# Performance work log

Measured on AMD Instinct MI355X. Metric: run time of the kernel, lower is better.

## Reference

```python
import jax, jax.numpy as jnp
import numpy as np

NUM_EMBEDDINGS = 512
EMBEDDING_DIM = 128
COMMITMENT = 0.25
DECAY = 0.99
EPS = 1e-05


def setup_inputs() -> dict:
    key = jax.random.key(0)
    k1, k2 = jax.random.split(key)
    z = jax.random.normal(k1, (32, EMBEDDING_DIM, 64, 64), dtype=jnp.float32)
    embedding = jax.random.normal(k2, (EMBEDDING_DIM, NUM_EMBEDDINGS), dtype=jnp.float32)
    cluster_size = jnp.zeros((NUM_EMBEDDINGS,), dtype=jnp.float32)
    embed_avg = embedding  # buffer initialized as a clone of embedding
    return {"z": z, "embedding": embedding, "cluster_size": cluster_size, "embed_avg": embed_avg}


def reference(z, embedding, cluster_size, embed_avg):
    sg = jax.lax.stop_gradient
    D, K = embedding.shape
    B, C, H, W = z.shape
    z_perm = jnp.transpose(z, (0, 2, 3, 1))          # [B,H,W,D]
    flat_z = z_perm.reshape(-1, D)                    # [N,D]

    distances = ((flat_z ** 2).sum(1, keepdims=True)
                 - 2.0 * (flat_z @ embedding)
                 + (embedding ** 2).sum(0)[None, :])  # [N,K]
    idx = jnp.argmin(distances, axis=1)               # [N]

    # gather codes (equivalent to one-hot @ embedding.T, without materializing one-hot)
    quantized = jnp.take(embedding.T, idx, axis=0).reshape(z_perm.shape)  # [B,H,W,D]
    quantized = jnp.transpose(quantized, (0, 3, 1, 2))                    # [B,D,H,W]

    # EMA codebook update (training branch)
    enc_sum = jax.ops.segment_sum(jnp.ones_like(idx, dtype=flat_z.dtype), idx, num_segments=K)  # [K]
    embed_sum = jax.ops.segment_sum(flat_z, idx, num_segments=K).T                              # [D,K]
    new_cluster_size = cluster_size * DECAY + (1.0 - DECAY) * enc_sum
    new_embed_avg = embed_avg * DECAY + (1.0 - DECAY) * embed_sum
    n = jnp.maximum(new_cluster_size.sum(), 1e-05)
    cs = (new_cluster_size + EPS) / (n + K * EPS) * n
    new_embedding = new_embed_avg / cs[None, :]

    e_latent_loss = jnp.mean((sg(quantized) - z) ** 2)
    q_latent_loss = jnp.mean((quantized - sg(z)) ** 2)
    loss = q_latent_loss + COMMITMENT * e_latent_loss

    quantized_out = z + sg(quantized - z)             # straight-through
    encoding_indices = idx.reshape(B, H, W)
    return (quantized_out, loss, encoding_indices, new_embedding, new_cluster_size, new_embed_avg)
```

## Files before the change

### kernel.cpp

```cpp
#include <hip/hip_runtime.h>
#include <hip/hip_bf16.h>
#include <float.h>

typedef _Float16 f16;
typedef __attribute__((ext_vector_type(8))) _Float16 half8;
typedef __attribute__((ext_vector_type(4))) float floatx4;

#define DIM   128
#define HW    4096
#define NPOS  131072
#define K     512
#define ZSTRIDE_B 524288

#define Q_OFF     0
#define LOSS_OFF  16777216
#define IDX_OFF   16777217
#define NEMB_OFF  16908289
#define NCS_OFF   16973825
#define NEA_OFF   16974337

#define WS_LOSS  0
#define WS_E2    2
#define WS_ENC   514
#define WS_ESUM  1026
#define WS_ZERO_COUNT 66562
#define WS_EHI   66564
#define WS_ELO   99332

#define XST 136

__global__ __launch_bounds__(256) void k_prep(const float* __restrict__ emb,
                                              f16* __restrict__ ehiP,
                                              f16* __restrict__ eloP,
                                              float* __restrict__ e2) {
    int lin = blockIdx.x * 256 + threadIdx.x;
    int o = lin >> 9, k = lin & 511;
    int g = k >> 4, r = k & 15;
    half8 hh, ll;
    float s = 0.f;
    #pragma unroll
    for (int j = 0; j < 8; ++j) {
        float v = emb[(o * 8 + j) * K + k];
        f16 h = (f16)v;
        f16 l = (f16)(v - (float)h);
        hh[j] = h; ll[j] = l;
        s = fmaf(v, v, s);
    }
    int base = (g * 4 + (o >> 2)) * 512 + (o & 3) * 128 + r * 8;
    *(half8*)&ehiP[base] = hh;
    *(half8*)&eloP[base] = ll;
    unsafeAtomicAdd(&e2[k], s);
}

__global__ __launch_bounds__(256) void k_assign(const float* __restrict__ z,
                                                const f16* __restrict__ ehiP,
                                                const f16* __restrict__ eloP,
                                                const float* __restrict__ e2,
                                                float* __restrict__ out,
                                                float* __restrict__ lossAcc) {
    __shared__ f16 xs_h[64 * XST];
    __shared__ f16 xs_l[64 * XST];
    __shared__ float wbD[256];
    __shared__ int   wbI[256];
    __shared__ int   bidx[64];
    __shared__ float wred[4];

    const int tid  = threadIdx.x;
    const int lane = tid & 63;
    const int wv   = tid >> 6;
    const int n0   = blockIdx.x * 64;
    const int b    = n0 >> 12;
    const int hw0  = n0 & 4095;
    const float* zb = z + b * ZSTRIDE_B + hw0;
    const int l15  = lane & 15;
    const int quad = lane >> 4;

    float sv0[16], sv1[16];
    #pragma unroll
    for (int it = 0; it < 16; ++it) {
        int lin = tid + it * 256;
        int i  = lin & 63;
        int dp = lin >> 6;
        sv0[it] = zb[(2 * dp) * HW + i];
        sv1[it] = zb[(2 * dp + 1) * HW + i];
    }
    #pragma unroll
    for (int it = 0; it < 16; ++it) {
        int lin = tid + it * 256;
        int i  = lin & 63;
        int dp = lin >> 6;
        float v0 = sv0[it], v1 = sv1[it];
        f16 h0 = (f16)v0; f16 l0 = (f16)(v0 - (float)h0);
        f16 h1 = (f16)v1; f16 l1 = (f16)(v1 - (float)h1);
        union { f16 h[2]; unsigned int u; } ph, pl;
        ph.h[0] = h0; ph.h[1] = h1;
        pl.h[0] = l0; pl.h[1] = l1;
        *(unsigned int*)&xs_h[i * XST + 2 * dp] = ph.u;
        *(unsigned int*)&xs_l[i * XST + 2 * dp] = pl.u;
    }
    __syncthreads();

    float bestD[4][4];
    int   bestI[4][4];
    #pragma unroll
    for (int t = 0; t < 4; ++t)
        #pragma unroll
        for (int r = 0; r < 4; ++r) { bestD[t][r] = FLT_MAX; bestI[t][r] = 0x7fffffff; }

    const half8* gh = (const half8*)ehiP;
    const half8* gl = (const half8*)eloP;

    for (int cc = 0; cc < 4; ++cc) {
        half8 Bh[4][2], Bl[4][2];
        #pragma unroll
        for (int dc = 0; dc < 4; ++dc)
            #pragma unroll
            for (int nt = 0; nt < 2; ++nt) {
                int g  = cc * 8 + wv * 2 + nt;
                int bi = (g * 4 + dc) * 64 + lane;
                Bh[dc][nt] = gh[bi];
                Bl[dc][nt] = gl[bi];
            }

        floatx4 acc[4][2];
        #pragma unroll
        for (int t = 0; t < 4; ++t)
            #pragma unroll
            for (int nt = 0; nt < 2; ++nt) acc[t][nt] = (floatx4){0.f, 0.f, 0.f, 0.f};

        #pragma unroll
        for (int dc = 0; dc < 4; ++dc) {
            half8 ah[4], al[4];
            #pragma unroll
            for (int t = 0; t < 4; ++t) {
                int off = (t * 16 + l15) * XST + dc * 32 + quad * 8;
                ah[t] = *(const half8*)&xs_h[off];
                al[t] = *(const half8*)&xs_l[off];
            }
            #pragma unroll
            for (int nt = 0; nt < 2; ++nt) {
                #pragma unroll
                for (int t = 0; t < 4; ++t) {
                    acc[t][nt] = __builtin_amdgcn_mfma_f32_16x16x32_f16(ah[t], Bh[dc][nt], acc[t][nt], 0, 0, 0);
                    acc[t][nt] = __builtin_amdgcn_mfma_f32_16x16x32_f16(al[t], Bh[dc][nt], acc[t][nt], 0, 0, 0);
                    acc[t][nt] = __builtin_amdgcn_mfma_f32_16x16x32_f16(ah[t], Bl[dc][nt], acc[t][nt], 0, 0, 0);
                }
            }
        }
        #pragma unroll
        for (int nt = 0; nt < 2; ++nt) {
            int c = cc * 128 + wv * 32 + nt * 16 + l15;
            float ee = e2[c];
            #pragma unroll
            for (int t = 0; t < 4; ++t)
                #pragma unroll
                for (int r = 0; r < 4; ++r) {
                    float s = fmaf(-2.f, acc[t][nt][r], ee);
                    if (s < bestD[t][r]) { bestD[t][r] = s; bestI[t][r] = c; }
                }
        }
    }

    #pragma unroll
    for (int mask = 1; mask <= 8; mask <<= 1) {
        #pragma unroll
        for (int t = 0; t < 4; ++t)
            #pragma unroll
            for (int r = 0; r < 4; ++r) {
                float od = __shfl_xor(bestD[t][r], mask, 64);
                int   oi = __shfl_xor(bestI[t][r], mask, 64);
                if (od < bestD[t][r] || (od == bestD[t][r] && oi < bestI[t][r])) {
                    bestD[t][r] = od; bestI[t][r] = oi;
                }
            }
    }
    if (l15 == 0) {
        #pragma unroll
        for (int t = 0; t < 4; ++t)
            #pragma unroll
            for (int r = 0; r < 4; ++r) {
                int m = t * 16 + quad * 4 + r;
                wbD[wv * 64 + m] = bestD[t][r];
                wbI[wv * 64 + m] = bestI[t][r];
            }
    }
    __syncthreads();
    if (tid < 64) {
        float bd = wbD[tid]; int bi = wbI[tid];
        #pragma unroll
        for (int w = 1; w < 4; ++w) {
            float od = wbD[w * 64 + tid]; int oi = wbI[w * 64 + tid];
            if (od < bd || (od == bd && oi < bi)) { bd = od; bi = oi; }
        }
        bidx[tid] = bi;
        out[IDX_OFF + n0 + tid] = (float)bi;
    }
    __syncthreads();

    float* qb = out + Q_OFF + b * ZSTRIDE_B + hw0;
    float lsum = 0.f;
    #pragma unroll
    for (int it = 0; it < 4; ++it) {
        int o = wv * 4 + it;
        int c = bidx[lane];
        int g = c >> 4, r = c & 15;
        int base = (g * 4 + (o >> 2)) * 512 + (o & 3) * 128 + r * 8;
        half8 hh = *(const half8*)&ehiP[base];
        half8 ll = *(const half8*)&eloP[base];
        half8 zh = *(const half8*)&xs_h[lane * XST + o * 8];
        half8 zl = *(const half8*)&xs_l[lane * XST + o * 8];
        #pragma unroll
        for (int jj = 0; jj < 8; ++jj) {
            float q  = (float)hh[jj] + (float)ll[jj];
            float zz = (float)zh[jj] + (float)zl[jj];
            qb[(o * 8 + jj) * HW + lane] = q;
            float df = q - zz;
            lsum = fmaf(df, df, lsum);
        }
    }
    #pragma unroll
    for (int m = 32; m >= 1; m >>= 1) lsum += __shfl_xor(lsum, m, 64);
    if (lane == 0) wred[wv] = lsum;
    __syncthreads();
    if (tid == 0) unsafeAtomicAdd(lossAcc, wred[0] + wred[1] + wred[2] + wred[3]);
}

#define DC 8
__global__ __launch_bounds__(256) void k_ema2(const float* __restrict__ z,
                                              const float* __restrict__ out,
                                              float* __restrict__ enc,
                                              float* __restrict__ esum) {
    __shared__ float acc[DC][K];
    __shared__ float cnt[K];

    const int tid = threadIdx.x;
    const int half   = blockIdx.x & 1;
    const int dchunk = (blockIdx.x >> 1) & 15;
    const int b      = blockIdx.x >> 5;
    const int d0 = dchunk * DC;
    const bool doCnt = (dchunk == 0);

    for (int i = tid; i < DC * K; i += 256) ((float*)acc)[i] = 0.f;
    if (doCnt) for (int i = tid; i < K; i += 256) cnt[i] = 0.f;
    __syncthreads();

    const float* zb  = z + b * ZSTRIDE_B;
    const float* idp = out + IDX_OFF + b * HW;

    const int p0 = half * 2048;
    for (int t = p0; t < p0 + 2048; t += 1024) {
        const int p = t + 4 * tid;
        float4 iv = *(const float4*)(idp + p);
        int k0 = (int)iv.x;
        int k1 = (int)iv.y;
        int k2 = (int)iv.z;
        int k3 = (int)iv.w;
        if (doCnt) {
            atomicAdd(&cnt[k0], 1.f); atomicAdd(&cnt[k1], 1.f);
            atomicAdd(&cnt[k2], 1.f); atomicAdd(&cnt[k3], 1.f);
        }
        #pragma unroll
        for (int d = 0; d < DC; ++d) {
            float4 zv = *(const float4*)(zb + (d0 + d) * HW + p);
            atomicAdd(&acc[d][k0], zv.x);
            atomicAdd(&acc[d][k1], zv.y);
            atomicAdd(&acc[d][k2], zv.z);
            atomicAdd(&acc[d][k3], zv.w);
        }
    }
    __syncthreads();

    const int rot = (blockIdx.x & 31) << 6;
    for (int i = tid; i < DC * K; i += 256) {
        int j = (i + rot) & (DC * K - 1);
        int d = j >> 9, k = j & 511;
        unsafeAtomicAdd(&esum[(d0 + d) * K + k], acc[d][k]);
    }
    if (doCnt) for (int i = tid; i < K; i += 256) unsafeAtomicAdd(&enc[i], cnt[i]);
}

__global__ __launch_bounds__(512) void k_final(const float* __restrict__ enc,
                                               const float* __restrict__ cs_in,
                                               const float* __restrict__ lossAcc,
                                               const float* __restrict__ esum,
                                               const float* __restrict__ eavg_in,
                                               float* __restrict__ out) {
    __shared__ float red[512];
    int k = threadIdx.x;
    int d = blockIdx.x;
    float ncs = fmaf(cs_in[k], 0.99f, 0.01f * enc[k]);
    red[k] = ncs;
    __syncthreads();
    for (int s = 256; s > 0; s >>= 1) {
        if (k < s) red[k] += red[k + s];
        __syncthreads();
    }
    float nn = fmaxf(red[0], 1e-5f);
    float cs = (ncs + 1e-5f) / (nn + (float)K * 1e-5f) * nn;
    float ea = fmaf(eavg_in[d * K + k], 0.99f, 0.01f * esum[d * K + k]);
    out[NEA_OFF + d * K + k] = ea;
    out[NEMB_OFF + d * K + k] = ea / cs;
    if (d == 0) {
        out[NCS_OFF + k] = ncs;
        if (k == 0) out[LOSS_OFF] = lossAcc[0] * 1.25f / 16777216.0f;
    }
}

extern "C" void kernel_launch(void* const* d_in, const int* in_sizes, int n_in,
                              void* d_out, int out_size, void* d_ws, size_t ws_size,
                              hipStream_t stream) {
    const float* z     = (const float*)d_in[0];
    const float* emb   = (const float*)d_in[1];
    const float* cs_in = (const float*)d_in[2];
    const float* eavg  = (const float*)d_in[3];
    float* out = (float*)d_out;
    float* wsF = (float*)d_ws;

    hipMemsetAsync(wsF, 0, WS_ZERO_COUNT * sizeof(float), stream);

    k_prep<<<32, 256, 0, stream>>>(emb, (f16*)(wsF + WS_EHI), (f16*)(wsF + WS_ELO),
                                   wsF + WS_E2);
    k_assign<<<NPOS / 64, 256, 0, stream>>>(z,
                                            (const f16*)(wsF + WS_EHI),
                                            (const f16*)(wsF + WS_ELO),
                                            wsF + WS_E2, out, wsF + WS_LOSS);
    k_ema2<<<1024, 256, 0, stream>>>(z, out, wsF + WS_ENC, wsF + WS_ESUM);
    k_final<<<128, 512, 0, stream>>>(wsF + WS_ENC, cs_in, wsF + WS_LOSS,
                                     wsF + WS_ESUM, eavg, out);
}
```

Baseline: 348.3 us.

## Software-pipeline codebook fragment loads and cap registers for two blocks per SIMD

```diff
diff --git a/kernel.cpp b/kernel.cpp
--- a/kernel.cpp
+++ b/kernel.cpp
@@ -52,12 +52,12 @@
     unsafeAtomicAdd(&e2[k], s);
 }
 
-__global__ __launch_bounds__(256) void k_assign(const float* __restrict__ z,
-                                                const f16* __restrict__ ehiP,
-                                                const f16* __restrict__ eloP,
-                                                const float* __restrict__ e2,
-                                                float* __restrict__ out,
-                                                float* __restrict__ lossAcc) {
+__global__ __launch_bounds__(256, 2) void k_assign(const float* __restrict__ z,
+                                                   const f16* __restrict__ ehiP,
+                                                   const f16* __restrict__ eloP,
+                                                   const float* __restrict__ e2,
+                                                   float* __restrict__ out,
+                                                   float* __restrict__ lossAcc) {
     __shared__ f16 xs_h[64 * XST];
     __shared__ f16 xs_l[64 * XST];
     __shared__ float wbD[256];
@@ -74,6 +74,17 @@
     const float* zb = z + b * ZSTRIDE_B + hw0;
     const int l15  = lane & 15;
     const int quad = lane >> 4;
+
+    const half8* gh = (const half8*)ehiP;
+    const half8* gl = (const half8*)eloP;
+
+    half8 bh[2], bl[2];
+    #pragma unroll
+    for (int nt = 0; nt < 2; ++nt) {
+        int g = wv * 2 + nt;
+        bh[nt] = gh[(g * 4 + 0) * 64 + lane];
+        bl[nt] = gl[(g * 4 + 0) * 64 + lane];
+    }
 
     float sv0[16], sv1[16];
     #pragma unroll
@@ -107,45 +118,45 @@
         #pragma unroll
         for (int r = 0; r < 4; ++r) { bestD[t][r] = FLT_MAX; bestI[t][r] = 0x7fffffff; }
 
-    const half8* gh = (const half8*)ehiP;
-    const half8* gl = (const half8*)eloP;
-
     for (int cc = 0; cc < 4; ++cc) {
-        half8 Bh[4][2], Bl[4][2];
-        #pragma unroll
-        for (int dc = 0; dc < 4; ++dc)
-            #pragma unroll
-            for (int nt = 0; nt < 2; ++nt) {
-                int g  = cc * 8 + wv * 2 + nt;
-                int bi = (g * 4 + dc) * 64 + lane;
-                Bh[dc][nt] = gh[bi];
-                Bl[dc][nt] = gl[bi];
+        floatx4 acc[4][2];
+        #pragma unroll
+        for (int t = 0; t < 4; ++t)
+            #pragma unroll
+            for (int nt = 0; nt < 2; ++nt) acc[t][nt] = (floatx4){0.f, 0.f, 0.f, 0.f};
+
+        #pragma unroll
+        for (int dc = 0; dc < 4; ++dc) {
+            half8 nbh[2], nbl[2];
+            if (dc < 3) {
+                #pragma unroll
+                for (int nt = 0; nt < 2; ++nt) {
+                    int g = cc * 8 + wv * 2 + nt;
+                    nbh[nt] = gh[(g * 4 + dc + 1) * 64 + lane];
+                    nbl[nt] = gl[(g * 4 + dc + 1) * 64 + lane];
+                }
+            } else if (cc < 3) {
+                #pragma unroll
+                for (int nt = 0; nt < 2; ++nt) {
+                    int g = (cc + 1) * 8 + wv * 2 + nt;
+                    nbh[nt] = gh[(g * 4 + 0) * 64 + lane];
+                    nbl[nt] = gl[(g * 4 + 0) * 64 + lane];
+                }
             }
-
-        floatx4 acc[4][2];
-        #pragma unroll
-        for (int t = 0; t < 4; ++t)
-            #pragma unroll
-            for (int nt = 0; nt < 2; ++nt) acc[t][nt] = (floatx4){0.f, 0.f, 0.f, 0.f};
-
-        #pragma unroll
-        for (int dc = 0; dc < 4; ++dc) {
-            half8 ah[4], al[4];
             #pragma unroll
             for (int t = 0; t < 4; ++t) {
                 int off = (t * 16 + l15) * XST + dc * 32 + quad * 8;
-                ah[t] = *(const half8*)&xs_h[off];
-                al[t] = *(const half8*)&xs_l[off];
+                half8 ah = *(const half8*)&xs_h[off];
+                half8 al = *(const half8*)&xs_l[off];
+                #pragma unroll
+                for (int nt = 0; nt < 2; ++nt) {
+                    acc[t][nt] = __builtin_amdgcn_mfma_f32_16x16x32_f16(ah, bh[nt], acc[t][nt], 0, 0, 0);
+                    acc[t][nt] = __builtin_amdgcn_mfma_f32_16x16x32_f16(al, bh[nt], acc[t][nt], 0, 0, 0);
+                    acc[t][nt] = __builtin_amdgcn_mfma_f32_16x16x32_f16(ah, bl[nt], acc[t][nt], 0, 0, 0);
+                }
             }
             #pragma unroll
-            for (int nt = 0; nt < 2; ++nt) {
-                #pragma unroll
-                for (int t = 0; t < 4; ++t) {
-                    acc[t][nt] = __builtin_amdgcn_mfma_f32_16x16x32_f16(ah[t], Bh[dc][nt], acc[t][nt], 0, 0, 0);
-                    acc[t][nt] = __builtin_amdgcn_mfma_f32_16x16x32_f16(al[t], Bh[dc][nt], acc[t][nt], 0, 0, 0);
-                    acc[t][nt] = __builtin_amdgcn_mfma_f32_16x16x32_f16(ah[t], Bl[dc][nt], acc[t][nt], 0, 0, 0);
-                }
-            }
+            for (int nt = 0; nt < 2; ++nt) { bh[nt] = nbh[nt]; bl[nt] = nbl[nt]; }
         }
         #pragma unroll
         for (int nt = 0; nt < 2; ++nt) {
```

Result: faster. 313.2 us (-10.1%).
